# Kernel optimization log

Hardware: AMD Instinct MI355X
Metric: run time of the kernel (lower is better)

## Reference

```python
import jax, jax.numpy as jnp
import numpy as np

CUBE_NEIGHBOR = jnp.array([[-1, 0, 0], [0, -1, 0], [0, 0, -1]], dtype=jnp.int64)


def setup_inputs() -> dict:
    key = jax.random.key(0)
    ks = jax.random.split(key, 6)
    k, F, H, O = 128, 64, 128, 2
    N_es = 200000
    topo_feat = jax.random.normal(ks[0], (k, k, k, F), dtype=jnp.float32)
    esid = jax.random.randint(ks[1], (N_es, 3), 0, k).astype(jnp.int64)
    W1 = jax.random.normal(ks[2], (2 * F, H), dtype=jnp.float32) * (1.0 / np.sqrt(2 * F))
    b1 = jnp.zeros((H,), dtype=jnp.float32)
    W2 = jax.random.normal(ks[3], (H, H), dtype=jnp.float32) * (1.0 / np.sqrt(H))
    b2 = jnp.zeros((H,), dtype=jnp.float32)
    W3 = jax.random.normal(ks[4], (H, O), dtype=jnp.float32) * (1.0 / np.sqrt(H))
    b3 = jnp.zeros((O,), dtype=jnp.float32)
    return {"topo_feat": topo_feat, "esid": esid, "W1": W1, "b1": b1,
            "W2": W2, "b2": b2, "W3": W3, "b3": b3, "k": k}


def reference(topo_feat, esid, W1, b1, W2, b2, W3, b3, k):
    N_es = esid.shape[0]
    F = topo_feat.shape[-1]
    # gather edge features: [N_es, F]
    edge_feat = topo_feat[esid[:, 0], esid[:, 1], esid[:, 2]]
    # clamped neighbor indices: [N_es, 3, 3]
    eid_nn = jnp.clip(esid[:, None, :] + CUBE_NEIGHBOR, 0, k - 1)
    # gather neighbor features: [N_es, 3, F]
    feat_nn = topo_feat[eid_nn[..., 0], eid_nn[..., 1], eid_nn[..., 2]]
    # CubeFaceNet: repeat edge feat across the 3 faces, concat -> [N_es, 3, 2F]
    feat = jnp.concatenate(
        [jnp.broadcast_to(edge_feat[:, None, :], (N_es, 3, F)), feat_nn], axis=-1)
    # MLP forward_simple: dense + ReLU stack
    h = jax.nn.relu(feat @ W1 + b1)
    h = jax.nn.relu(h @ W2 + b2)
    out_face = h @ W3 + b3                     # [N_es, 3, 2]
    out_face = jnp.swapaxes(out_face, 1, 2)    # [N_es, 2, 3]
    # predict_type == 'Softmax' -> softmax over class dim (dim=1)
    return jax.nn.softmax(out_face, axis=1)
```

## Files before the change

kernel.cpp:

```cpp
#include <hip/hip_runtime.h>

typedef __attribute__((ext_vector_type(8))) short s16x8;
typedef __attribute__((ext_vector_type(16))) float f32x16;

#define THREADS 512
#define TROWS 32
#define RPB (8 * TROWS)
#define WS 152

__device__ __forceinline__ short f2bf(float f) {
    unsigned u = __float_as_uint(f);
    u += 0x7fffu + ((u >> 16) & 1u);
    return (short)(u >> 16);
}

__device__ __forceinline__ unsigned cvt_pk(float lo, float hi) {
    unsigned r;
    asm("v_cvt_pk_bf16_f32 %0, %1, %2" : "=v"(r) : "v"(lo), "v"(hi));
    return r;
}

__device__ __forceinline__ int kperm(int k) {
    int j = ((k >> 4) & 1) * 4 + ((k >> 1) & 3);
    return (k >> 5) * 32 + (j >> 1) * 8 + (j & 1) * 2 + ((k >> 3) & 1) * 4 + (k & 1);
}

__device__ __forceinline__ int wswz(int c, int k) {
    int g = k >> 3;
    int gs = (g < 16) ? (g ^ ((c >> 3) & 15)) : g;
    return c * WS + gs * 8 + (k & 7);
}

__device__ __forceinline__ s16x8 pack8(float4 a, float4 b) {
    union { unsigned u[4]; s16x8 v; } z;
    z.u[0] = cvt_pk(a.x, a.y); z.u[1] = cvt_pk(a.z, a.w);
    z.u[2] = cvt_pk(b.x, b.y); z.u[3] = cvt_pk(b.z, b.w);
    return z.v;
}

__launch_bounds__(THREADS, 2)
__global__ void edgeface_kernel(
    const float* __restrict__ topo, const int* __restrict__ esid,
    const float* __restrict__ W1, const float* __restrict__ b1,
    const float* __restrict__ W2, const float* __restrict__ b2,
    const float* __restrict__ W3, const float* __restrict__ b3,
    float* __restrict__ out, int nRows, int kg)
{
    __shared__ __align__(16) short sW1t[128 * WS];
    __shared__ __align__(16) short sW2t[128 * WS];
    __shared__ __align__(16) short sW3t[32 * WS];

    const int tid = threadIdx.x;

    for (int e = tid; e < 128 * WS; e += THREADS) {
        int c = e & 127, kk = e >> 7;
        float v1 = (kk < 128) ? W1[kk * 128 + c] : ((kk == 128) ? b1[c] : 0.f);
        float v2 = (kk < 128) ? W2[kperm(kk) * 128 + c] : ((kk == 128) ? b2[c] : 0.f);
        int d = wswz(c, kk);
        sW1t[d] = f2bf(v1);
        sW2t[d] = f2bf(v2);
    }
    for (int e = tid; e < 32 * WS; e += THREADS) {
        int c = e & 31, kk = e >> 5;
        float v = 0.f;
        if (c == 0) {
            if (kk < 128) {
                int p = kperm(kk);
                v = W3[p * 2 + 1] - W3[p * 2 + 0];
            } else if (kk == 128) {
                v = b3[1] - b3[0];
            }
        }
        sW3t[wswz(c, kk)] = f2bf(v);
    }
    __syncthreads();

    const int w = tid >> 6, lane = tid & 63;
    const int c31 = lane & 31;
    const int h   = lane >> 5;

    union { unsigned u[4]; s16x8 v; } za;
    za.u[0] = (h == 0) ? 0x00003F80u : 0u;
    za.u[1] = 0u; za.u[2] = 0u; za.u[3] = 0u;
    const s16x8 bfaug = za.v;

    const int G = gridDim.x;
    const int nTiles = (nRows + RPB - 1) / RPB;

    int e0, e1, e2;
    {
        int R = min(blockIdx.x * RPB + w * TROWS + c31, nRows - 1);
        int n = R / 3;
        e0 = esid[n * 3 + 0]; e1 = esid[n * 3 + 1]; e2 = esid[n * 3 + 2];
    }

    float4 pf[16];
    {
        int R = min(blockIdx.x * RPB + w * TROWS + c31, nRows - 1);
        int f = R - 3 * (R / 3);
        long ea = (((long)e0 * kg + e1) * kg + e2) * 64;
        long na = ((((long)((f == 0) ? max(e0 - 1, 0) : e0)) * kg
                  + ((f == 1) ? max(e1 - 1, 0) : e1)) * kg
                  + ((f == 2) ? max(e2 - 1, 0) : e2)) * 64;
        const float4* pe = (const float4*)(topo + ea);
        const float4* pn = (const float4*)(topo + na);
        #pragma unroll
        for (int ks = 0; ks < 4; ++ks) {
            pf[2 * ks + 0] = pe[ks * 4 + h * 2 + 0];
            pf[2 * ks + 1] = pe[ks * 4 + h * 2 + 1];
            pf[8 + 2 * ks + 0] = pn[ks * 4 + h * 2 + 0];
            pf[8 + 2 * ks + 1] = pn[ks * 4 + h * 2 + 1];
        }
        int Rn = min((blockIdx.x + G) * RPB + w * TROWS + c31, nRows - 1);
        int nn = Rn / 3;
        e0 = esid[nn * 3 + 0]; e1 = esid[nn * 3 + 1]; e2 = esid[nn * 3 + 2];
    }

    for (int tI = blockIdx.x; tI < nTiles; tI += G) {
        const int base = tI * RPB + w * TROWS;

        s16x8 bf[8];
        #pragma unroll
        for (int ks = 0; ks < 4; ++ks) {
            bf[ks]     = pack8(pf[2 * ks], pf[2 * ks + 1]);
            bf[4 + ks] = pack8(pf[8 + 2 * ks], pf[8 + 2 * ks + 1]);
        }

        {
            int Rn = min((tI + G) * RPB + w * TROWS + c31, nRows - 1);
            int f = Rn - 3 * (Rn / 3);
            long ea = (((long)e0 * kg + e1) * kg + e2) * 64;
            long na = ((((long)((f == 0) ? max(e0 - 1, 0) : e0)) * kg
                      + ((f == 1) ? max(e1 - 1, 0) : e1)) * kg
                      + ((f == 2) ? max(e2 - 1, 0) : e2)) * 64;
            const float4* pe = (const float4*)(topo + ea);
            const float4* pn = (const float4*)(topo + na);
            #pragma unroll
            for (int ks = 0; ks < 4; ++ks) {
                pf[2 * ks + 0] = pe[ks * 4 + h * 2 + 0];
                pf[2 * ks + 1] = pe[ks * 4 + h * 2 + 1];
                pf[8 + 2 * ks + 0] = pn[ks * 4 + h * 2 + 0];
                pf[8 + 2 * ks + 1] = pn[ks * 4 + h * 2 + 1];
            }
        }
        {
            int Rn = min((tI + 2 * G) * RPB + w * TROWS + c31, nRows - 1);
            int nn = Rn / 3;
            e0 = esid[nn * 3 + 0]; e1 = esid[nn * 3 + 1]; e2 = esid[nn * 3 + 2];
        }

        unsigned pk[4][8];
        #pragma unroll
        for (int n = 0; n < 4; ++n) {
            f32x16 c = {0.f,0.f,0.f,0.f,0.f,0.f,0.f,0.f,0.f,0.f,0.f,0.f,0.f,0.f,0.f,0.f};
            #pragma unroll
            for (int ks = 0; ks < 8; ++ks) {
                s16x8 af = *(const s16x8*)(sW1t + wswz(n * 32 + c31, ks * 16 + h * 8));
                c = __builtin_amdgcn_mfma_f32_32x32x16_bf16(af, bf[ks], c, 0, 0, 0);
            }
            {
                s16x8 af = *(const s16x8*)(sW1t + wswz(n * 32 + c31, 128 + h * 8));
                c = __builtin_amdgcn_mfma_f32_32x32x16_bf16(af, bfaug, c, 0, 0, 0);
            }
            #pragma unroll
            for (int j = 0; j < 8; ++j)
                pk[n][j] = cvt_pk(fmaxf(c[2 * j + 0], 0.f), fmaxf(c[2 * j + 1], 0.f));
        }

        unsigned pk2[4][8];
        #pragma unroll
        for (int n2 = 0; n2 < 4; ++n2) {
            f32x16 c = {0.f,0.f,0.f,0.f,0.f,0.f,0.f,0.f,0.f,0.f,0.f,0.f,0.f,0.f,0.f,0.f};
            #pragma unroll
            for (int ks = 0; ks < 8; ++ks) {
                s16x8 af = *(const s16x8*)(sW2t + wswz(n2 * 32 + c31, ks * 16 + h * 8));
                union { unsigned u[4]; s16x8 v; } bb;
                bb.u[0] = pk[ks >> 1][(ks & 1) * 4 + 0];
                bb.u[1] = pk[ks >> 1][(ks & 1) * 4 + 1];
                bb.u[2] = pk[ks >> 1][(ks & 1) * 4 + 2];
                bb.u[3] = pk[ks >> 1][(ks & 1) * 4 + 3];
                c = __builtin_amdgcn_mfma_f32_32x32x16_bf16(af, bb.v, c, 0, 0, 0);
            }
            {
                s16x8 af = *(const s16x8*)(sW2t + wswz(n2 * 32 + c31, 128 + h * 8));
                c = __builtin_amdgcn_mfma_f32_32x32x16_bf16(af, bfaug, c, 0, 0, 0);
            }
            #pragma unroll
            for (int j = 0; j < 8; ++j)
                pk2[n2][j] = cvt_pk(fmaxf(c[2 * j + 0], 0.f), fmaxf(c[2 * j + 1], 0.f));
        }

        f32x16 c3 = {0.f,0.f,0.f,0.f,0.f,0.f,0.f,0.f,0.f,0.f,0.f,0.f,0.f,0.f,0.f,0.f};
        #pragma unroll
        for (int ks = 0; ks < 8; ++ks) {
            s16x8 af = *(const s16x8*)(sW3t + wswz(c31, ks * 16 + h * 8));
            union { unsigned u[4]; s16x8 v; } bb;
            bb.u[0] = pk2[ks >> 1][(ks & 1) * 4 + 0];
            bb.u[1] = pk2[ks >> 1][(ks & 1) * 4 + 1];
            bb.u[2] = pk2[ks >> 1][(ks & 1) * 4 + 2];
            bb.u[3] = pk2[ks >> 1][(ks & 1) * 4 + 3];
            c3 = __builtin_amdgcn_mfma_f32_32x32x16_bf16(af, bb.v, c3, 0, 0, 0);
        }
        {
            s16x8 af = *(const s16x8*)(sW3t + wswz(c31, 128 + h * 8));
            c3 = __builtin_amdgcn_mfma_f32_32x32x16_bf16(af, bfaug, c3, 0, 0, 0);
        }

        float sel = c3[0];
        float dd = sel + __shfl_xor(sel, 32, 64);
        float p = 1.f / (1.f + __expf(h ? -dd : dd));
        int R = base + c31;
        if (R < nRows) {
            int n = R / 3, ff = R - 3 * n;
            out[n * 6 + h * 3 + ff] = p;
        }
    }
}

extern "C" void kernel_launch(void* const* d_in, const int* in_sizes, int n_in,
                              void* d_out, int out_size, void* d_ws, size_t ws_size,
                              hipStream_t stream) {
    const float* topo = (const float*)d_in[0];
    const int*   esid = (const int*)d_in[1];
    const float* W1 = (const float*)d_in[2];
    const float* b1 = (const float*)d_in[3];
    const float* W2 = (const float*)d_in[4];
    const float* b2 = (const float*)d_in[5];
    const float* W3 = (const float*)d_in[6];
    const float* b3 = (const float*)d_in[7];
    float* out = (float*)d_out;

    int nRows = in_sizes[1];
    int H = in_sizes[3];
    int F = (in_sizes[2] / H) / 2;
    long vol = (long)in_sizes[0] / F;
    int kg = 1;
    while ((long)(kg + 1) * (kg + 1) * (kg + 1) <= vol) ++kg;

    if (nRows <= 0) return;
    edgeface_kernel<<<dim3(256), dim3(THREADS), 0, stream>>>(
        topo, esid, W1, b1, W2, b2, W3, b3, out, nRows, kg);
}
```

Before: 75.17 us.

## Raise to 12 waves per block, shrink W3 LDS, interleave layer-3 MFMA

Raises the block to 768 threads (12 waves) with launch bounds for 3 blocks per CU, and shrinks the layer-3 weight tile in LDS from 32 rows to a single row plus a zero region that lanes other than the first read from. Layer-3 MFMAs are interleaved into the layer-2 loop so only one n2 slice of packed activations is live at a time, reducing register pressure. Layer-1 compute is moved ahead of the next tile's gather prefetch. The aim is more resident waves per CU to hide gather latency, at the risk of register spilling under the tighter launch bound and LDS capacity limiting the third block.

Result: slower. 113.8 us (+51.4%).

```diff
diff --git a/kernel.cpp b/kernel.cpp
--- a/kernel.cpp
+++ b/kernel.cpp
@@ -3,9 +3,10 @@
 typedef __attribute__((ext_vector_type(8))) short s16x8;
 typedef __attribute__((ext_vector_type(16))) float f32x16;
 
-#define THREADS 512
+#define THREADS 768
+#define WAVES 12
 #define TROWS 32
-#define RPB (8 * TROWS)
+#define RPB (WAVES * TROWS)
 #define WS 152
 
 __device__ __forceinline__ short f2bf(float f) {
@@ -38,7 +39,7 @@
     return z.v;
 }
 
-__launch_bounds__(THREADS, 2)
+__launch_bounds__(THREADS, 3)
 __global__ void edgeface_kernel(
     const float* __restrict__ topo, const int* __restrict__ esid,
     const float* __restrict__ W1, const float* __restrict__ b1,
@@ -48,7 +49,7 @@
 {
     __shared__ __align__(16) short sW1t[128 * WS];
     __shared__ __align__(16) short sW2t[128 * WS];
-    __shared__ __align__(16) short sW3t[32 * WS];
+    __shared__ __align__(16) short sW3t[WS + 8];
 
     const int tid = threadIdx.x;
 
@@ -60,18 +61,16 @@
         sW1t[d] = f2bf(v1);
         sW2t[d] = f2bf(v2);
     }
-    for (int e = tid; e < 32 * WS; e += THREADS) {
-        int c = e & 31, kk = e >> 5;
+    for (int e = tid; e < WS + 8; e += THREADS) {
+        int kk = e;
         float v = 0.f;
-        if (c == 0) {
-            if (kk < 128) {
-                int p = kperm(kk);
-                v = W3[p * 2 + 1] - W3[p * 2 + 0];
-            } else if (kk == 128) {
-                v = b3[1] - b3[0];
-            }
-        }
-        sW3t[wswz(c, kk)] = f2bf(v);
+        if (kk < 128) {
+            int p = kperm(kk);
+            v = W3[p * 2 + 1] - W3[p * 2 + 0];
+        } else if (kk == 128) {
+            v = b3[1] - b3[0];
+        }
+        sW3t[(kk < 144) ? wswz(0, kk) : kk] = f2bf(v);
     }
     __syncthreads();
 
@@ -83,6 +82,9 @@
     za.u[0] = (h == 0) ? 0x00003F80u : 0u;
     za.u[1] = 0u; za.u[2] = 0u; za.u[3] = 0u;
     const s16x8 bfaug = za.v;
+
+    const short* w3row = sW3t;
+    const short* w3zero = sW3t + 144;
 
     const int G = gridDim.x;
     const int nTiles = (nRows + RPB - 1) / RPB;
@@ -126,6 +128,24 @@
             bf[4 + ks] = pack8(pf[8 + 2 * ks], pf[8 + 2 * ks + 1]);
         }
 
+        unsigned pk[4][8];
+        #pragma unroll
+        for (int n = 0; n < 4; ++n) {
+            f32x16 c = {0.f,0.f,0.f,0.f,0.f,0.f,0.f,0.f,0.f,0.f,0.f,0.f,0.f,0.f,0.f,0.f};
+            #pragma unroll
+            for (int ks = 0; ks < 8; ++ks) {
+                s16x8 af = *(const s16x8*)(sW1t + wswz(n * 32 + c31, ks * 16 + h * 8));
+                c = __builtin_amdgcn_mfma_f32_32x32x16_bf16(af, bf[ks], c, 0, 0, 0);
+            }
+            {
+                s16x8 af = *(const s16x8*)(sW1t + wswz(n * 32 + c31, 128 + h * 8));
+                c = __builtin_amdgcn_mfma_f32_32x32x16_bf16(af, bfaug, c, 0, 0, 0);
+            }
+            #pragma unroll
+            for (int j = 0; j < 8; ++j)
+                pk[n][j] = cvt_pk(fmaxf(c[2 * j + 0], 0.f), fmaxf(c[2 * j + 1], 0.f));
+        }
+
         {
             int Rn = min((tI + G) * RPB + w * TROWS + c31, nRows - 1);
             int f = Rn - 3 * (Rn / 3);
@@ -149,25 +169,7 @@
             e0 = esid[nn * 3 + 0]; e1 = esid[nn * 3 + 1]; e2 = esid[nn * 3 + 2];
         }
 
-        unsigned pk[4][8];
-        #pragma unroll
-        for (int n = 0; n < 4; ++n) {
-            f32x16 c = {0.f,0.f,0.f,0.f,0.f,0.f,0.f,0.f,0.f,0.f,0.f,0.f,0.f,0.f,0.f,0.f};
-            #pragma unroll
-            for (int ks = 0; ks < 8; ++ks) {
-                s16x8 af = *(const s16x8*)(sW1t + wswz(n * 32 + c31, ks * 16 + h * 8));
-                c = __builtin_amdgcn_mfma_f32_32x32x16_bf16(af, bf[ks], c, 0, 0, 0);
-            }
-            {
-                s16x8 af = *(const s16x8*)(sW1t + wswz(n * 32 + c31, 128 + h * 8));
-                c = __builtin_amdgcn_mfma_f32_32x32x16_bf16(af, bfaug, c, 0, 0, 0);
-            }
-            #pragma unroll
-            for (int j = 0; j < 8; ++j)
-                pk[n][j] = cvt_pk(fmaxf(c[2 * j + 0], 0.f), fmaxf(c[2 * j + 1], 0.f));
-        }
-
-        unsigned pk2[4][8];
+        f32x16 c3 = {0.f,0.f,0.f,0.f,0.f,0.f,0.f,0.f,0.f,0.f,0.f,0.f,0.f,0.f,0.f,0.f};
         #pragma unroll
         for (int n2 = 0; n2 < 4; ++n2) {
             f32x16 c = {0.f,0.f,0.f,0.f,0.f,0.f,0.f,0.f,0.f,0.f,0.f,0.f,0.f,0.f,0.f,0.f};
@@ -185,24 +187,26 @@
                 s16x8 af = *(const s16x8*)(sW2t + wswz(n2 * 32 + c31, 128 + h * 8));
                 c = __builtin_amdgcn_mfma_f32_32x32x16_bf16(af, bfaug, c, 0, 0, 0);
             }
+            unsigned pk2[8];
             #pragma unroll
             for (int j = 0; j < 8; ++j)
-                pk2[n2][j] = cvt_pk(fmaxf(c[2 * j + 0], 0.f), fmaxf(c[2 * j + 1], 0.f));
-        }
-
-        f32x16 c3 = {0.f,0.f,0.f,0.f,0.f,0.f,0.f,0.f,0.f,0.f,0.f,0.f,0.f,0.f,0.f,0.f};
-        #pragma unroll
-        for (int ks = 0; ks < 8; ++ks) {
-            s16x8 af = *(const s16x8*)(sW3t + wswz(c31, ks * 16 + h * 8));
-            union { unsigned u[4]; s16x8 v; } bb;
-            bb.u[0] = pk2[ks >> 1][(ks & 1) * 4 + 0];
-            bb.u[1] = pk2[ks >> 1][(ks & 1) * 4 + 1];
-            bb.u[2] = pk2[ks >> 1][(ks & 1) * 4 + 2];
-            bb.u[3] = pk2[ks >> 1][(ks & 1) * 4 + 3];
-            c3 = __builtin_amdgcn_mfma_f32_32x32x16_bf16(af, bb.v, c3, 0, 0, 0);
+                pk2[j] = cvt_pk(fmaxf(c[2 * j + 0], 0.f), fmaxf(c[2 * j + 1], 0.f));
+            #pragma unroll
+            for (int half = 0; half < 2; ++half) {
+                int ks3 = 2 * n2 + half;
+                const short* ap = c31 ? w3zero : (w3row + wswz(0, ks3 * 16 + h * 8));
+                s16x8 af = *(const s16x8*)ap;
+                union { unsigned u[4]; s16x8 v; } bb;
+                bb.u[0] = pk2[half * 4 + 0];
+                bb.u[1] = pk2[half * 4 + 1];
+                bb.u[2] = pk2[half * 4 + 2];
+                bb.u[3] = pk2[half * 4 + 3];
+                c3 = __builtin_amdgcn_mfma_f32_32x32x16_bf16(af, bb.v, c3, 0, 0, 0);
+            }
         }
         {
-            s16x8 af = *(const s16x8*)(sW3t + wswz(c31, 128 + h * 8));
+            const short* ap = c31 ? w3zero : (w3row + wswz(0, 128 + h * 8));
+            s16x8 af = *(const s16x8*)ap;
             c3 = __builtin_amdgcn_mfma_f32_32x32x16_bf16(af, bfaug, c3, 0, 0, 0);
         }
 
```
